# Performance work log

Hardware: AMD Instinct MI355X
Metric: run time of the kernel (lower is better)

## Reference

```python
import jax, jax.numpy as jnp
import numpy as np

B, TE, TD, DE, DD, U = 32, 1024, 64, 512, 512, 512
REMOVE_FACTOR = 1000000.0


def setup_inputs() -> dict:
    key = jax.random.key(0)
    k = jax.random.split(key, 7)
    return {
        "en_seq": jax.random.normal(k[0], (B, TE, DE), jnp.float32),
        "de_seq": jax.random.normal(k[1], (B, TD, DD), jnp.float32),
        "mask": jax.random.randint(k[2], (B, TE), 0, 2).astype(jnp.int32),
        # W_h is a 1x1 conv [1,1,DE,U] == dense [DE,U]; w_c is [1,1,1,U] == vector [U]
        "W_h": jax.random.normal(k[3], (DE, U), jnp.float32) / np.float32(np.sqrt(DE)),
        "W_s": jax.random.normal(k[4], (DD, U), jnp.float32) / np.float32(np.sqrt(DD)),
        "w_c": jax.random.normal(k[5], (U,), jnp.float32) * np.float32(0.05),
        "v": jax.random.normal(k[6], (U,), jnp.float32) / np.float32(np.sqrt(U)),
    }


def reference(en_seq, de_seq, mask, W_h, W_s, w_c, v):
    m_en = mask.astype(en_seq.dtype)                      # [B,TE]
    en = en_seq * m_en[:, :, None]                        # masked encoder states
    enc_feat = jnp.einsum('bte,eu->btu', en, W_h)         # 1x1 conv == dense, [B,TE,U]
    dec_feat = jnp.einsum('bsd,du->bsu', de_seq, W_s)     # [B,TD,U]
    mask_bias = (m_en - 1.0) * REMOVE_FACTOR              # masked_attention additive bias

    def step(coverage, df):
        # coverage: [B,TE]; df: [B,U]
        feat = jnp.tanh(enc_feat + df[:, None, :] + coverage[:, :, None] * w_c)  # [B,TE,U]
        mu = jnp.einsum('btu,u->bt', feat, v) + mask_bias                        # [B,TE]
        alpha = jax.nn.softmax(mu, axis=-1)                                      # [B,TE]
        ctx = jnp.einsum('bt,bte->be', alpha, en)                                # [B,DE]
        covloss = jnp.minimum(coverage, alpha)                                   # [B,TE]
        return coverage + alpha, (ctx, alpha, covloss)

    cov0 = jnp.zeros(en_seq.shape[:2], en_seq.dtype)
    _, (ctx, alphas, covlosses) = jax.lax.scan(step, cov0, jnp.swapaxes(dec_feat, 0, 1))
    ctx = jnp.swapaxes(ctx, 0, 1)                # [B,TD,DE]
    output = jnp.concatenate([de_seq, ctx], -1)  # [B,TD,DD+DE]
    return output, jnp.swapaxes(alphas, 0, 1), jnp.swapaxes(covlosses, 0, 1)
```

## Files before the change

kernel.cpp:

```cpp
#include <hip/hip_runtime.h>
#include <float.h>

#define B   32
#define TE  1024
#define TD  64
#define DE  512
#define DD  512
#define U   512
#define K   512
#define NB  8
#define RPB 128

#if __has_builtin(__builtin_amdgcn_exp2f)
#define EXP2F __builtin_amdgcn_exp2f
#else
#define EXP2F exp2f
#endif
#if __has_builtin(__builtin_amdgcn_rcpf)
#define RCPF __builtin_amdgcn_rcpf
#else
#define RCPF(x) (1.0f / (x))
#endif

#define TANH_C 2.8853900817779268f
#define L2E    1.4426950408889634f

typedef __attribute__((ext_vector_type(8))) short bf16x8;
typedef __attribute__((ext_vector_type(4))) float f32x4;

__device__ __forceinline__ float wave_reduce_sum(float v) {
    #pragma unroll
    for (int o = 32; o; o >>= 1) v += __shfl_xor(v, o, 64);
    return v;
}

__device__ __forceinline__ unsigned short f2bf(float f) {
    unsigned u = __float_as_uint(f);
    unsigned r = (u + 0x7fffu + ((u >> 16) & 1u)) >> 16;
    return (unsigned short)r;
}
__device__ __forceinline__ float bflo(unsigned x) { return __uint_as_float(x << 16); }
__device__ __forceinline__ float bfhi(unsigned x) { return __uint_as_float(x & 0xffff0000u); }
__device__ __forceinline__ void unpack8(uint4 q, float* f) {
    f[0] = bflo(q.x); f[1] = bfhi(q.x); f[2] = bflo(q.y); f[3] = bfhi(q.y);
    f[4] = bflo(q.z); f[5] = bfhi(q.z); f[6] = bflo(q.w); f[7] = bfhi(q.w);
}

__device__ __forceinline__ unsigned long long ld_agent64(const unsigned long long* p) {
    return __hip_atomic_load(p, __ATOMIC_RELAXED, __HIP_MEMORY_SCOPE_AGENT);
}
__device__ __forceinline__ void st_agent64(unsigned long long* p, unsigned long long v) {
    __hip_atomic_store(p, v, __ATOMIC_RELAXED, __HIP_MEMORY_SCOPE_AGENT);
}

#define LBAR() do { \
    asm volatile("s_waitcnt lgkmcnt(0)" ::: "memory"); \
    __builtin_amdgcn_s_barrier(); \
    __builtin_amdgcn_sched_barrier(0); \
} while (0)

__global__ __launch_bounds__(256) void k_prep(
        const float4* __restrict__ en_seq, ushort4* __restrict__ en_bf,
        const float4* __restrict__ de_seq, ushort4* __restrict__ de_bf,
        float4* __restrict__ outp,
        const float* __restrict__ W_h, unsigned short* __restrict__ Wh_t,
        const float* __restrict__ W_s, unsigned short* __restrict__ Ws_t,
        unsigned long long* __restrict__ stats)
{
    __shared__ float t[64][65];
    const int tid = threadIdx.x;
    for (int blk = blockIdx.x; blk < 18562; blk += 2048) {
        if (blk < 16384) {
            size_t i = (size_t)blk * 256 + tid;
            float4 f = en_seq[i];
            ushort4 r; r.x = f2bf(f.x); r.y = f2bf(f.y); r.z = f2bf(f.z); r.w = f2bf(f.w);
            en_bf[i] = r;
        } else if (blk < 17408) {
            size_t i = (size_t)(blk - 16384) * 256 + tid;
            float4 f = de_seq[i];
            ushort4 r; r.x = f2bf(f.x); r.y = f2bf(f.y); r.z = f2bf(f.z); r.w = f2bf(f.w);
            de_bf[i] = r;
        } else if (blk < 18432) {
            size_t i = (size_t)(blk - 17408) * 256 + tid;
            size_t r = i >> 7, c = i & 127;
            outp[r * 256 + c] = de_seq[i];
        } else if (blk < 18560) {
            int id = blk - 18432;
            const float* W = (id < 64) ? W_h : W_s;
            unsigned short* Wt = (id < 64) ? Wh_t : Ws_t;
            int bid = id & 63;
            const int bx = bid & 7, by = bid >> 3;
            const int lx = tid & 63, ly = tid >> 6;
            #pragma unroll
            for (int i = 0; i < 64; i += 4)
                t[ly + i][lx] = W[(size_t)(by * 64 + ly + i) * 512 + bx * 64 + lx];
            __syncthreads();
            #pragma unroll
            for (int i = 0; i < 64; i += 4)
                Wt[(size_t)(bx * 64 + ly + i) * 512 + by * 64 + lx] = f2bf(t[lx][ly + i]);
        } else {
            int i = (blk - 18560) * 256 + tid;
            stats[i] = 0ull;
        }
    }
}

__global__ __launch_bounds__(256) void k_mfma(
        const unsigned short* __restrict__ Ae, const unsigned short* __restrict__ Be,
        unsigned short* __restrict__ Ce,
        const unsigned short* __restrict__ Ad, const unsigned short* __restrict__ Bd,
        unsigned short* __restrict__ Cd)
{
    const int tid = threadIdx.x;
    const int w = tid >> 6, lane = tid & 63;
    const int quad = lane >> 4, l16 = lane & 15;
    const short* A; const short* Bt; unsigned short* C; int mb;
    if (blockIdx.y < 256) {
        A = (const short*)Ae; Bt = (const short*)Be; C = Ce; mb = blockIdx.y * 128;
    } else {
        A = (const short*)Ad; Bt = (const short*)Bd; C = Cd; mb = (blockIdx.y - 256) * 128;
    }
    const int m0 = mb + (w >> 1) * 64;
    const int n0 = blockIdx.x * 128 + (w & 1) * 64;

    const short* Ab = A  + (size_t)(m0 + l16) * K + quad * 8;
    const short* Bb = Bt + (size_t)(n0 + l16) * K + quad * 8;

    f32x4 acc[4][4] = {};
    for (int ks = 0; ks < K; ks += 32) {
        bf16x8 af[4], bg[4];
        #pragma unroll
        for (int i = 0; i < 4; i++)
            af[i] = *(const bf16x8*)(Ab + (size_t)i * 16 * K + ks);
        #pragma unroll
        for (int j = 0; j < 4; j++)
            bg[j] = *(const bf16x8*)(Bb + (size_t)j * 16 * K + ks);
        #pragma unroll
        for (int i = 0; i < 4; i++)
            #pragma unroll
            for (int j = 0; j < 4; j++)
                acc[i][j] = __builtin_amdgcn_mfma_f32_16x16x32_bf16(
                    af[i], bg[j], acc[i][j], 0, 0, 0);
    }
    #pragma unroll
    for (int i = 0; i < 4; i++)
        #pragma unroll
        for (int j = 0; j < 4; j++)
            #pragma unroll
            for (int r = 0; r < 4; r++) {
                int m = m0 + i * 16 + quad * 4 + r;
                int n = n0 + j * 16 + l16;
                C[(size_t)m * U + n] = f2bf(acc[i][j][r]);
            }
}

__global__ __launch_bounds__(1024, 4) void k_scan(
        const unsigned short* __restrict__ enc_bf,
        const unsigned short* __restrict__ dec_bf,
        const unsigned short* en_bf,
        const float* __restrict__ w_c,
        const float* __restrict__ v,
        const int* __restrict__ mask,
        unsigned long long* __restrict__ stats,
        float* pctx,
        float* __restrict__ out)
{
    const int blk = blockIdx.x;
    const int b = blk & 31, g = blk >> 5;
    const int tid = threadIdx.x;
    const int w = tid >> 6, lane = tid & 63;
    const int u = lane * 8;

    __shared__ __align__(16) unsigned short s_enc[RPB * U];
    __shared__ __align__(16) float s_p[RPB];
    __shared__ float  s_cov[RPB];
    __shared__ short  s_rowid[RPB];
    __shared__ unsigned long long s_bal[16];
    __shared__ float  s_wsum[16];
    __shared__ float  s_q[4][512];
    __shared__ float  s_inv;

    const int* maskb = mask + b * TE;
    float* alphas = out + (size_t)B * TD * (DD + DE);
    float* covl   = alphas + (size_t)B * TD * TE;

    float wcc[8], vv[8], vsuml;
    {
        float4 a0 = *(const float4*)&w_c[u];
        float4 a1 = *(const float4*)&w_c[u + 4];
        wcc[0]=a0.x*TANH_C; wcc[1]=a0.y*TANH_C; wcc[2]=a0.z*TANH_C; wcc[3]=a0.w*TANH_C;
        wcc[4]=a1.x*TANH_C; wcc[5]=a1.y*TANH_C; wcc[6]=a1.z*TANH_C; wcc[7]=a1.w*TANH_C;
        float4 b0 = *(const float4*)&v[u];
        float4 b1 = *(const float4*)&v[u + 4];
        vv[0]=b0.x; vv[1]=b0.y; vv[2]=b0.z; vv[3]=b0.w;
        vv[4]=b1.x; vv[5]=b1.y; vv[6]=b1.z; vv[7]=b1.w;
        vsuml = ((vv[0]+vv[1])+(vv[2]+vv[3])) + ((vv[4]+vv[5])+(vv[6]+vv[7]));
    }

    int act = (maskb[tid] != 0);
    {
        unsigned long long bal = __ballot(act);
        if (lane == 0) s_bal[w] = bal;
        if (tid < RPB) { s_p[tid] = 0.f; s_cov[tid] = 0.f; s_rowid[tid] = 0; }
        __syncthreads();
    }
    int nact = 0, pre = 0;
    {
        #pragma unroll
        for (int ww = 0; ww < 16; ww++) {
            int c = __popcll(s_bal[ww]);
            if (ww < w) pre += c;
            nact += c;
        }
        pre += __popcll(s_bal[w] & ((1ull << lane) - 1));
        if (act && (pre & 7) == g) s_rowid[pre >> 3] = (short)tid;
    }
    const int Sblk = (nact + 7 - g) >> 3;

    for (int t = tid; t < RPB * TD; t += 1024) {
        int rl = t & 127, s = t >> 7;
        if (maskb[g * RPB + rl] == 0) {
            size_t rowo = ((size_t)b * TD + s) * TE + g * RPB + rl;
            alphas[rowo] = 0.f;
            covl[rowo]   = 0.f;
        }
    }
    __syncthreads();

    {
        const int slot = tid >> 3, part = tid & 7;
        const uint4* src = (const uint4*)
            (enc_bf + ((size_t)b * TE + s_rowid[slot]) * U);
        uint4* dst = (uint4*)(s_enc + (size_t)slot * U);
        #pragma unroll
        for (int j = 0; j < 8; j++) dst[part + j * 8] = src[part + j * 8];
    }
    const int e2 = tid & 255, q4 = tid >> 8;
    unsigned enreg[32];
    {
        const unsigned* enw = (const unsigned*)en_bf;
        #pragma unroll
        for (int r = 0; r < 32; r++) {
            int row = s_rowid[q4 * 32 + r];
            enreg[r] = enw[((size_t)b * TE + row) * (DE / 2) + e2];
        }
    }
    float* myctx = pctx + ((size_t)b * 1024 + g * RPB) * 256;

    __syncthreads();

    uint4 qd = *(const uint4*)(dec_bf + ((size_t)b * TD) * U + u);

    float inv_prev = 0.f;
    for (int s = 0; s < TD; s++) {
        float dfc[8];
        unpack8(qd, dfc);
        #pragma unroll
        for (int j = 0; j < 8; j++) dfc[j] *= TANH_C;

        float local_esum = 0.f;
        for (int i = w; i < Sblk; i += 16) {
            float pold   = s_p[i];
            float covold = s_cov[i];
            float aprev  = pold * inv_prev;
            float cov    = covold + aprev;
            if (s > 0 && lane == 0) {
                size_t rowo = ((size_t)b * TD + (s - 1)) * TE + s_rowid[i];
                alphas[rowo] = aprev;
                covl[rowo]   = fminf(covold, aprev);
            }
            uint4 q = *(const uint4*)(s_enc + (size_t)i * U + u);
            float e[8]; unpack8(q, e);
            float acc2 = 0.f;
            #pragma unroll
            for (int j = 0; j < 8; j++) {
                float arg = fmaf(cov, wcc[j], fmaf(e[j], TANH_C, dfc[j]));
                acc2 = fmaf(vv[j], RCPF(EXP2F(arg) + 1.0f), acc2);
            }
            float part = fmaf(acc2, -2.0f, vsuml);
            part = wave_reduce_sum(part);
            float pe = EXP2F(part * L2E);
            if (lane == 0) { s_p[i] = pe; s_cov[i] = cov; }
            local_esum += pe;
        }
        if (lane == 0) s_wsum[w] = local_esum;

        LBAR();

        unsigned long long* sl = stats + ((size_t)(s & 1) * B + b) * NB;
        if (w == 0) {
            float x = (lane < 16) ? s_wsum[lane] : 0.f;
            x += __shfl_xor(x, 8, 64);
            x += __shfl_xor(x, 4, 64);
            x += __shfl_xor(x, 2, 64);
            x += __shfl_xor(x, 1, 64);
            if (lane == 0) {
                unsigned long long pv =
                    ((unsigned long long)__float_as_uint(x) << 32) |
                    (unsigned)(s + 1);
                st_agent64(&sl[g], pv);
            }
        }

        {
            int sn = (s + 1 < TD) ? s + 1 : s;
            qd = *(const uint4*)(dec_bf + (((size_t)b * TD + sn) * U + u));
        }

        {
            const float4* pb = (const float4*)&s_p[q4 * 32];
            float a0 = 0.f, a1 = 0.f;
            #pragma unroll
            for (int k = 0; k < 8; k++) {
                float4 pp = pb[k];
                a0 = fmaf(pp.x, bflo(enreg[4*k]),   a0);
                a1 = fmaf(pp.x, bfhi(enreg[4*k]),   a1);
                a0 = fmaf(pp.y, bflo(enreg[4*k+1]), a0);
                a1 = fmaf(pp.y, bfhi(enreg[4*k+1]), a1);
                a0 = fmaf(pp.z, bflo(enreg[4*k+2]), a0);
                a1 = fmaf(pp.z, bfhi(enreg[4*k+2]), a1);
                a0 = fmaf(pp.w, bflo(enreg[4*k+3]), a0);
                a1 = fmaf(pp.w, bfhi(enreg[4*k+3]), a1);
            }
            s_q[q4][2 * e2]     = a0;
            s_q[q4][2 * e2 + 1] = a1;
        }

        if (w == 0) {
            unsigned long long pv = 0;
            for (;;) {
                if (lane < NB) pv = ld_agent64(&sl[lane]);
                unsigned long long okm =
                    __ballot(lane < NB ? ((unsigned)pv == (unsigned)(s + 1)) : 1);
                if (~okm == 0ull) break;
                __builtin_amdgcn_s_sleep(1);
            }
            float tg = (lane < NB) ? __uint_as_float((unsigned)(pv >> 32)) : 0.f;
            tg = wave_reduce_sum(tg);
            if (lane == 0) s_inv = RCPF(tg);
        }

        LBAR();

        inv_prev = s_inv;

        if (tid < 512) {
            float ts = s_q[0][tid] + s_q[1][tid] + s_q[2][tid] + s_q[3][tid];
            myctx[(size_t)s * 512 + tid] = ts * inv_prev;
        }
    }

    for (int i = w; i < Sblk; i += 16) {
        if (lane == 0) {
            float aprev = s_p[i] * inv_prev;
            size_t rowo = ((size_t)b * TD + (TD - 1)) * TE + s_rowid[i];
            alphas[rowo] = aprev;
            covl[rowo]   = fminf(s_cov[i], aprev);
        }
    }
}

__global__ __launch_bounds__(1024) void k_ctx(
        const float* __restrict__ pctx, float* __restrict__ out)
{
    for (int idx = blockIdx.x * 1024 + threadIdx.x; idx < 1048576;
         idx += 256 * 1024) {
        int b = idx >> 15, rem = idx & 32767;
        const float* p = pctx + (size_t)b * 262144 + rem;
        float t = 0.f;
        #pragma unroll
        for (int g = 0; g < NB; g++) t += p[(size_t)g * 32768];
        int s = rem >> 9, e = rem & 511;
        out[((size_t)b * TD + s) * (DD + DE) + DD + e] = t;
    }
}

extern "C" void kernel_launch(void* const* d_in, const int* in_sizes, int n_in,
                              void* d_out, int out_size, void* d_ws, size_t ws_size,
                              hipStream_t stream) {
    const float* en_seq = (const float*)d_in[0];
    const float* de_seq = (const float*)d_in[1];
    const int*   mask   = (const int*)d_in[2];
    const float* W_h    = (const float*)d_in[3];
    const float* W_s    = (const float*)d_in[4];
    const float* w_c    = (const float*)d_in[5];
    const float* v      = (const float*)d_in[6];
    float* out = (float*)d_out;

    unsigned short* enc_bf = (unsigned short*)d_ws;
    unsigned short* en_bf  = enc_bf + (size_t)B * TE * U;
    unsigned short* dec_bf = en_bf  + (size_t)B * TE * DE;
    unsigned short* Wh_t   = dec_bf + (size_t)B * TD * U;
    unsigned short* de_bf  = Wh_t   + (size_t)K * U;
    unsigned short* Ws_t   = de_bf  + (size_t)B * TD * DD;
    unsigned long long* stats =
        (unsigned long long*)(Ws_t + (size_t)K * U);
    float* pctx = (float*)en_bf;

    k_prep<<<2048, 256, 0, stream>>>((const float4*)en_seq, (ushort4*)en_bf,
                                     (const float4*)de_seq, (ushort4*)de_bf,
                                     (float4*)out, W_h, Wh_t, W_s, Ws_t, stats);
    k_mfma<<<dim3(4, 272), 256, 0, stream>>>(en_bf, Wh_t, enc_bf,
                                             de_bf, Ws_t, dec_bf);

    void* args[] = { (void*)&enc_bf, (void*)&dec_bf, (void*)&en_bf,
                     (void*)&w_c, (void*)&v, (void*)&mask,
                     (void*)&stats, (void*)&pctx, (void*)&out };
    hipLaunchCooperativeKernel((const void*)k_scan, dim3(256), dim3(1024),
                               args, 0, stream);

    k_ctx<<<256, 1024, 0, stream>>>(pctx, out);
}
```

Measured before the change: 544.6 us.

## Pre-tile bf16 operands into MFMA fragment layout for contiguous wave loads

```diff
diff --git a/kernel.cpp b/kernel.cpp
--- a/kernel.cpp
+++ b/kernel.cpp
@@ -28,6 +28,7 @@
 typedef __attribute__((ext_vector_type(8))) short bf16x8;
 typedef __attribute__((ext_vector_type(4))) float f32x4;
 
+
 __device__ __forceinline__ float wave_reduce_sum(float v) {
     #pragma unroll
     for (int o = 32; o; o >>= 1) v += __shfl_xor(v, o, 64);
@@ -60,47 +61,65 @@
 } while (0)
 
 __global__ __launch_bounds__(256) void k_prep(
-        const float4* __restrict__ en_seq, ushort4* __restrict__ en_bf,
-        const float4* __restrict__ de_seq, ushort4* __restrict__ de_bf,
+        const float* __restrict__ en_seq, unsigned short* __restrict__ en_bf,
+        const float* __restrict__ de_seq, unsigned short* __restrict__ de_bf,
         float4* __restrict__ outp,
         const float* __restrict__ W_h, unsigned short* __restrict__ Wh_t,
         const float* __restrict__ W_s, unsigned short* __restrict__ Ws_t,
         unsigned long long* __restrict__ stats)
 {
-    __shared__ float t[64][65];
+    __shared__ __align__(16) unsigned char sbuf[16640];
     const int tid = threadIdx.x;
-    for (int blk = blockIdx.x; blk < 18562; blk += 2048) {
-        if (blk < 16384) {
-            size_t i = (size_t)blk * 256 + tid;
-            float4 f = en_seq[i];
-            ushort4 r; r.x = f2bf(f.x); r.y = f2bf(f.y); r.z = f2bf(f.z); r.w = f2bf(f.w);
-            en_bf[i] = r;
-        } else if (blk < 17408) {
-            size_t i = (size_t)(blk - 16384) * 256 + tid;
-            float4 f = de_seq[i];
-            ushort4 r; r.x = f2bf(f.x); r.y = f2bf(f.y); r.z = f2bf(f.z); r.w = f2bf(f.w);
-            de_bf[i] = r;
-        } else if (blk < 18432) {
-            size_t i = (size_t)(blk - 17408) * 256 + tid;
+    for (int vb = blockIdx.x; vb < 3329; vb += 2048) {
+        if (vb < 2176) {
+            const float* src; unsigned short* dst; int rb;
+            if (vb < 2048) { src = en_seq; dst = en_bf; rb = vb; }
+            else           { src = de_seq; dst = de_bf; rb = vb - 2048; }
+            unsigned short* tbl = (unsigned short*)sbuf;
+            const float4* s4 = (const float4*)(src + (size_t)rb * 8192);
+            #pragma unroll
+            for (int i = 0; i < 8; i++) {
+                int idx = tid + i * 256;
+                float4 f = s4[idx];
+                ushort4 r; r.x = f2bf(f.x); r.y = f2bf(f.y);
+                r.z = f2bf(f.z); r.w = f2bf(f.w);
+                *(ushort4*)&tbl[(idx >> 7) * 520 + (idx & 127) * 4] = r;
+            }
+            __syncthreads();
+            uint4* d4 = (uint4*)(dst + (size_t)rb * 8192);
+            #pragma unroll
+            for (int i = 0; i < 4; i++) {
+                int c = tid + i * 256;
+                d4[c] = *(const uint4*)&tbl[(c & 15) * 520 + (c >> 4) * 8];
+            }
+            __syncthreads();
+        } else if (vb < 3200) {
+            size_t i = (size_t)(vb - 2176) * 256 + tid;
             size_t r = i >> 7, c = i & 127;
-            outp[r * 256 + c] = de_seq[i];
-        } else if (blk < 18560) {
-            int id = blk - 18432;
+            outp[r * 256 + c] = ((const float4*)de_seq)[i];
+        } else if (vb < 3328) {
+            int id = vb - 3200;
             const float* W = (id < 64) ? W_h : W_s;
             unsigned short* Wt = (id < 64) ? Wh_t : Ws_t;
             int bid = id & 63;
             const int bx = bid & 7, by = bid >> 3;
             const int lx = tid & 63, ly = tid >> 6;
+            float* t = (float*)sbuf;
             #pragma unroll
             for (int i = 0; i < 64; i += 4)
-                t[ly + i][lx] = W[(size_t)(by * 64 + ly + i) * 512 + bx * 64 + lx];
+                t[(ly + i) * 65 + lx] =
+                    W[(size_t)(by * 64 + ly + i) * 512 + bx * 64 + lx];
             __syncthreads();
             #pragma unroll
-            for (int i = 0; i < 64; i += 4)
-                Wt[(size_t)(bx * 64 + ly + i) * 512 + by * 64 + lx] = f2bf(t[lx][ly + i]);
+            for (int i = 0; i < 64; i += 4) {
+                int n = bx * 64 + ly + i, k = by * 64 + lx;
+                Wt[((size_t)(n >> 4) * 64 + (k >> 3)) * 128
+                   + (n & 15) * 8 + (k & 7)] = f2bf(t[lx * 65 + ly + i]);
+            }
+            __syncthreads();
         } else {
-            int i = (blk - 18560) * 256 + tid;
-            stats[i] = 0ull;
+            stats[tid] = 0ull;
+            stats[tid + 256] = 0ull;
         }
     }
 }
@@ -123,18 +142,19 @@
     const int m0 = mb + (w >> 1) * 64;
     const int n0 = blockIdx.x * 128 + (w & 1) * 64;
 
-    const short* Ab = A  + (size_t)(m0 + l16) * K + quad * 8;
-    const short* Bb = Bt + (size_t)(n0 + l16) * K + quad * 8;
+    const short* Ab = A  + (size_t)(m0 >> 4) * 64 * 128 + l16 * 8;
+    const short* Bb = Bt + (size_t)(n0 >> 4) * 64 * 128 + l16 * 8;
 
     f32x4 acc[4][4] = {};
     for (int ks = 0; ks < K; ks += 32) {
+        const int kc = (ks >> 3) + quad;
         bf16x8 af[4], bg[4];
         #pragma unroll
         for (int i = 0; i < 4; i++)
-            af[i] = *(const bf16x8*)(Ab + (size_t)i * 16 * K + ks);
+            af[i] = *(const bf16x8*)(Ab + ((size_t)i * 64 + kc) * 128);
         #pragma unroll
         for (int j = 0; j < 4; j++)
-            bg[j] = *(const bf16x8*)(Bb + (size_t)j * 16 * K + ks);
+            bg[j] = *(const bf16x8*)(Bb + ((size_t)j * 64 + kc) * 128);
         #pragma unroll
         for (int i = 0; i < 4; i++)
             #pragma unroll
@@ -241,8 +261,9 @@
         const unsigned* enw = (const unsigned*)en_bf;
         #pragma unroll
         for (int r = 0; r < 32; r++) {
-            int row = s_rowid[q4 * 32 + r];
-            enreg[r] = enw[((size_t)b * TE + row) * (DE / 2) + e2];
+            int rg = b * TE + s_rowid[q4 * 32 + r];
+            enreg[r] = enw[((size_t)(rg >> 4) * 64 + (e2 >> 2)) * 64
+                           + (rg & 15) * 4 + (e2 & 3)];
         }
     }
     float* myctx = pctx + ((size_t)b * 1024 + g * RPB) * 256;
@@ -397,8 +418,7 @@
         (unsigned long long*)(Ws_t + (size_t)K * U);
     float* pctx = (float*)en_bf;
 
-    k_prep<<<2048, 256, 0, stream>>>((const float4*)en_seq, (ushort4*)en_bf,
-                                     (const float4*)de_seq, (ushort4*)de_bf,
+    k_prep<<<2048, 256, 0, stream>>>(en_seq, en_bf, de_seq, de_bf,
                                      (float4*)out, W_h, Wh_t, W_s, Ws_t, stats);
     k_mfma<<<dim3(4, 272), 256, 0, stream>>>(en_bf, Wh_t, enc_bf,
                                              de_bf, Ws_t, dec_bf);
```

Result: faster. 514.4 us (-5.6%).
